# Performance work log

Measured on AMD Instinct MI355X. Metric: run time of the kernel, lower is better.

The kernel has to match this reference:

```python
import jax, jax.numpy as jnp
import numpy as np

N_AGENTS = 8
N_ENEMIES = 8
N_ALLIES = 7
H = 64            # rnn_hidden_dim (must be 64: Encoder latent dim hardcoded to 64, fed to fc3)
HEADS = 2         # hpn_head_num
OUT_NORMAL = 6    # output_normal_actions
N_ACTIONS = OUT_NORMAL + N_ENEMIES  # 14, required by expand_as in original code
E_DIM = 8
A_DIM = 8
OWN_DIM = 30
HYPER = 64        # hpn_hyper_dim
ENC_HID = 128     # predict_net_dim
BS = 2048


def _gru_cell(x, h, Wih, Whh, bih, bhh):
    # torch GRUCell math, gate order (r, z, n)
    gi = x @ Wih + bih
    gh = h @ Whh + bhh
    ir, iz, inn = jnp.split(gi, 3, axis=-1)
    hr, hz, hn = jnp.split(gh, 3, axis=-1)
    r = jax.nn.sigmoid(ir + hr)
    z = jax.nn.sigmoid(iz + hz)
    n = jnp.tanh(inn + r * hn)
    return (1.0 - z) * n + z * h


def setup_inputs() -> dict:
    key = jax.random.key(0)
    ks = jax.random.split(key, 48)
    B = BS * N_AGENTS

    def w(k, shape):
        return jax.random.normal(k, shape, dtype=jnp.float32) * 0.05

    he_out = ((E_DIM + 1) * H + 1) * HEADS   # 1154
    ha_out = A_DIM * H * HEADS               # 1024 (non-MMM map)

    return {
        "bs": BS,
        "own_feats": jax.random.normal(ks[0], (B, OWN_DIM), jnp.float32),
        "enemy_feats": jax.random.normal(ks[1], (B * N_ENEMIES, E_DIM), jnp.float32),
        "ally_feats": jax.random.normal(ks[2], (B * N_ALLIES, A_DIM), jnp.float32),
        "agent_ids": jax.random.randint(ks[3], (B,), 0, N_AGENTS),
        "last_action_ids": jax.random.randint(ks[4], (B,), 0, N_ACTIONS),
        "hidden_state": jax.random.normal(ks[5], (B, H), jnp.float32) * 0.1,
        "fc1_own_W": w(ks[6], (OWN_DIM, H)), "fc1_own_b": w(ks[7], (H,)),
        "agent_emb": w(ks[8], (N_AGENTS, H)),
        "action_emb": w(ks[9], (N_ACTIONS, H)),
        "he_W1": w(ks[10], (E_DIM, HYPER)), "he_b1": w(ks[11], (HYPER,)),
        "he_W2": w(ks[12], (HYPER, he_out)), "he_b2": w(ks[13], (he_out,)),
        "ha_W1": w(ks[14], (A_DIM, HYPER)), "ha_b1": w(ks[15], (HYPER,)),
        "ha_W2": w(ks[16], (HYPER, ha_out)), "ha_b2": w(ks[17], (ha_out,)),
        "merger_in_w": jnp.ones((1, HEADS, H), jnp.float32),
        "merger_out_w": jnp.ones((1, HEADS, 1), jnp.float32),
        "gru_Wih": w(ks[18], (H, 3 * H)), "gru_Whh": w(ks[19], (H, 3 * H)),
        "gru_bih": w(ks[20], (3 * H,)), "gru_bhh": w(ks[21], (3 * H,)),
        "fc2n_W": w(ks[22], (H, OUT_NORMAL)), "fc2n_b": w(ks[23], (OUT_NORMAL,)),
        "fc1b_W": w(ks[24], (OWN_DIM, H)), "fc1b_b": w(ks[25], (H,)),
        "gru2_Wih": w(ks[26], (H, 3 * H)), "gru2_Whh": w(ks[27], (H, 3 * H)),
        "gru2_bih": w(ks[28], (3 * H,)), "gru2_bhh": w(ks[29], (3 * H,)),
        "enc_W1": w(ks[30], (H, ENC_HID)), "enc_b1": w(ks[31], (ENC_HID,)),
        "enc_W2": w(ks[32], (ENC_HID, H)), "enc_b2": w(ks[33], (H,)),
        "fc3_W": w(ks[34], (H, N_ACTIONS)), "fc3_b": w(ks[35], (N_ACTIONS,)),
        "mlp_W": w(ks[36], (N_AGENTS, H, N_ACTIONS)), "mlp_b": w(ks[37], (N_AGENTS, N_ACTIONS)),
    }


def reference(bs, own_feats, enemy_feats, ally_feats, agent_ids, last_action_ids,
              hidden_state, fc1_own_W, fc1_own_b, agent_emb, action_emb,
              he_W1, he_b1, he_W2, he_b2, ha_W1, ha_b1, ha_W2, ha_b2,
              merger_in_w, merger_out_w, gru_Wih, gru_Whh, gru_bih, gru_bhh,
              fc2n_W, fc2n_b, fc1b_W, fc1b_b, gru2_Wih, gru2_Whh, gru2_bih, gru2_bhh,
              enc_W1, enc_b1, enc_W2, enc_b2, fc3_W, fc3_b, mlp_W, mlp_b):
    B = bs * N_AGENTS

    # own embedding + id/action embeddings
    emb_own = own_feats @ fc1_own_W + fc1_own_b
    emb_own = emb_own + agent_emb[agent_ids] + action_emb[last_action_ids]

    # hypernet-generated per-enemy fc1 weights, applied per entity, summed over enemies
    he = jax.nn.relu(enemy_feats @ he_W1 + he_b1) @ he_W2 + he_b2  # [B*E, 1154]
    cut = (H + 1) * HEADS
    w1e = he[:, :-cut].reshape(-1, E_DIM, H * HEADS)               # [B*E, e_dim, H*heads]
    emb_en = jnp.einsum('nd,ndk->nk', enemy_feats, w1e)
    emb_en = emb_en.reshape(B, N_ENEMIES, HEADS, H).sum(axis=1)    # [B, heads, H]

    ha = jax.nn.relu(ally_feats @ ha_W1 + ha_b1) @ ha_W2 + ha_b2   # [B*A, 1024]
    w1a = ha.reshape(-1, A_DIM, H * HEADS)
    emb_al = jnp.einsum('nd,ndk->nk', ally_feats, w1a)
    emb_al = emb_al.reshape(B, N_ALLIES, HEADS, H).sum(axis=1)     # [B, heads, H]

    # Merger over heads (softmax-weighted sum)
    mw = jax.nn.softmax(merger_in_w, axis=1)                       # [1, heads, H]
    merged = jnp.sum(mw * (emb_en + emb_al), axis=1)               # [B, H]

    x = jax.nn.relu(emb_own + merged)
    hh = _gru_cell(x, hidden_state, gru_Wih, gru_Whh, gru_bih, gru_bhh)  # [B, H]

    q_normal = (hh @ fc2n_W + fc2n_b).reshape(bs, N_AGENTS, OUT_NORMAL)

    # hypernet-generated attack output heads
    w2 = he[:, -cut:-HEADS].reshape(B, N_ENEMIES, H, HEADS)
    w2 = w2.transpose(0, 2, 1, 3).reshape(B, H, N_ENEMIES * HEADS)
    b2 = he[:, -HEADS:].reshape(B, N_ENEMIES * HEADS)
    qa = jnp.einsum('bh,bhk->bk', hh, w2) + b2                     # [B, E*heads]
    qa = qa.reshape(B * N_ENEMIES, HEADS)
    mo = jax.nn.softmax(merger_out_w[:, :, 0], axis=1)             # [1, heads]
    q_attack = jnp.sum(mo * qa, axis=1).reshape(bs, N_AGENTS, N_ENEMIES)

    q = jnp.concatenate([q_normal, q_attack], axis=-1)             # [bs, n_agents, 14]

    # parallel fc1 -> single-step GRU -> encoder branch
    x2 = jax.nn.relu(own_feats @ fc1b_W + fc1b_b)                  # [B, H]
    g = _gru_cell(x2, hidden_state, gru2_Wih, gru2_Whh, gru2_bih, gru2_bhh)  # [B, H]
    z = jax.nn.relu(g @ enc_W1 + enc_b1) @ enc_W2 + enc_b2         # [B, 64] encoder latent
    q_f = (z @ fc3_W + fc3_b).reshape(bs, N_AGENTS, N_ACTIONS)

    # per-agent mlps applied to first n_agents rows of gru output (as in original)
    ga = g[:N_AGENTS]                                              # [n_agents, H]
    local_q = jnp.einsum('ah,ahk->ak', ga, mlp_W) + mlp_b          # [n_agents, n_actions]
    local_qe = jnp.broadcast_to(local_q[None], q.shape)

    q_total = q + local_qe + q_f
    return (q_total, hh.reshape(bs, N_AGENTS, H), local_qe, q_f)
```

## Files before the change

kernel.cpp:

```cpp
#include <hip/hip_runtime.h>

#define HH_OFF 229376
#define LQE_OFF 1277952
#define QF_OFF 1507328

#define WB_HE 0
#define WB_HA 17408
#define WS_ATT 34816
#define WS_BATT 38912
#define WS_BH 38976
#define WS_BC 39040
#define WS_LQ 39056
#define WS_G1 39168
#define WS_G2 63744
#define WS_E1 88320
#define WS_E2 96512
#define WS_F1 104704
#define WS_END 108800

#define AWAVE 2448
#define ASAMP 336
#define TA_SH 552
#define BSTR 384

using s8v = __attribute__((ext_vector_type(8))) short;
using f4v = __attribute__((ext_vector_type(4))) float;

struct Params {
  const float *own, *ef, *af, *hid;
  const int *aid, *lid;
  const float *fc1oW, *fc1ob, *aemb, *actemb;
  const float *heW1, *heb1, *heW2, *heb2;
  const float *haW1, *hab1, *haW2, *hab2;
  const float *mi, *mo;
  const float *gWih, *gWhh, *gbih, *gbhh;
  const float *fc2nW, *fc2nb;
  const float *fc1bW, *fc1bb;
  const float *g2Wih, *g2Whh, *g2bih, *g2bhh;
  const float *eW1, *eb1, *eW2, *eb2;
  const float *fc3W, *fc3b;
  const float *mlpW, *mlpb;
};

__device__ __forceinline__ float sigm(float x) {
  x = fminf(fmaxf(x, -30.f), 30.f);
  return 1.f / (1.f + __expf(-x));
}
__device__ __forceinline__ float tanh_(float x) {
  x = fminf(fmaxf(x, -15.f), 15.f);
  float e = __expf(-2.f * x);
  return (1.f - e) / (1.f + e);
}
__device__ __forceinline__ unsigned short f2bf(float f) {
  unsigned u = __float_as_uint(f);
  return (unsigned short)((u + 0x7FFFu + ((u >> 16) & 1u)) >> 16);
}

__device__ __forceinline__ float hefold(const Params& p, int t, int h, float mw0, float mw1) {
  if (t < 512) {
    int d = t >> 6, j = t & 63;
    return mw0 * p.heW2[j * 1154 + d * 128 + h] + mw1 * p.heW2[j * 1154 + d * 128 + 64 + h];
  }
  if (t < 520) {
    int d = t - 512;
    return mw0 * p.heb2[d * 128 + h] + mw1 * p.heb2[d * 128 + 64 + h];
  }
  return 0.f;
}
__device__ __forceinline__ float hafold(const Params& p, int t, int h, float mw0, float mw1) {
  if (t < 512) {
    int d = t >> 6, j = t & 63;
    return mw0 * p.haW2[j * 1024 + d * 128 + h] + mw1 * p.haW2[j * 1024 + d * 128 + 64 + h];
  }
  if (t < 520) {
    int d = t - 512;
    return mw0 * p.hab2[d * 128 + h] + mw1 * p.hab2[d * 128 + 64 + h];
  }
  return 0.f;
}

__global__ void __launch_bounds__(512) prep_kernel(Params p, float* __restrict__ ws) {
  const int tid = threadIdx.x;
  if (blockIdx.x == 0) {
    __shared__ float g8[8][64];
    __shared__ float x2s[8][64];
    const int w = __builtin_amdgcn_readfirstlane(tid >> 6);
    const int lane = tid & 63;
    {
      float acc = p.fc1bb[lane];
      const float* ow = p.own + w * 30;
      for (int d = 0; d < 30; ++d) acc += ow[d] * p.fc1bW[d * 64 + lane];
      x2s[w][lane] = fmaxf(acc, 0.f);
      float a0 = p.g2bih[lane], a1 = p.g2bih[64 + lane], a2 = p.g2bih[128 + lane];
      float b0 = p.g2bhh[lane], b1 = p.g2bhh[64 + lane], b2 = p.g2bhh[128 + lane];
      const float* hidw = p.hid + w * 64;
      for (int k = 0; k < 64; ++k) {
        float xk = x2s[w][k];
        float hk = hidw[k];
        a0 += xk * p.g2Wih[k * 192 + lane];
        a1 += xk * p.g2Wih[k * 192 + 64 + lane];
        a2 += xk * p.g2Wih[k * 192 + 128 + lane];
        b0 += hk * p.g2Whh[k * 192 + lane];
        b1 += hk * p.g2Whh[k * 192 + 64 + lane];
        b2 += hk * p.g2Whh[k * 192 + 128 + lane];
      }
      float r = sigm(a0 + b0), z = sigm(a1 + b1);
      float n = tanh_(a2 + r * b2);
      g8[w][lane] = (1.f - z) * n + z * hidw[lane];
    }
    __syncthreads();
    if (tid < 112) {
      int a = tid / 14, c = tid % 14;
      float lacc = p.mlpb[a * 14 + c];
      for (int h = 0; h < 64; ++h) lacc += g8[a][h] * p.mlpW[(a * 64 + h) * 14 + c];
      ws[WS_LQ + tid] = lacc;
    }
    return;
  }
  const int idx = (int)(blockIdx.x - 1) * 512 + tid;
  if (idx >= WS_END) return;
  const float mo0 = sigm(p.mo[0] - p.mo[1]);
  const float mo1 = 1.f - mo0;
  if (idx < 34816) {
    int rel = (idx < WB_HA) ? idx : idx - WB_HA;
    int jp = rel & 3, lane = (rel >> 2) & 63, rest = rel >> 8;
    int nc = rest & 3, ks = rest >> 2;
    int t0 = ks * 32 + ((lane >> 4) << 3) + jp * 2;
    int h = nc * 16 + (lane & 15);
    float mw0 = sigm(p.mi[h] - p.mi[64 + h]);
    float mw1 = 1.f - mw0;
    float v0, v1;
    if (idx < WB_HA) {
      v0 = hefold(p, t0, h, mw0, mw1);
      v1 = hefold(p, t0 + 1, h, mw0, mw1);
    } else {
      v0 = hafold(p, t0, h, mw0, mw1);
      v1 = hafold(p, t0 + 1, h, mw0, mw1);
    }
    unsigned pk = (unsigned)f2bf(v0) | ((unsigned)f2bf(v1) << 16);
    ws[idx] = __uint_as_float(pk);
  } else if (idx < 38912) {
    int rel = idx - WS_ATT;
    int c = rel >> 8, rem = rel & 255, j = rem >> 2, q = rel & 3;
    int h = c * 4 + q;
    ws[idx] = mo0 * p.heW2[j * 1154 + 1024 + 2 * h] + mo1 * p.heW2[j * 1154 + 1024 + 2 * h + 1];
  } else if (idx < 38976) {
    int j = idx - WS_BATT;
    ws[idx] = mo0 * p.heW2[j * 1154 + 1152] + mo1 * p.heW2[j * 1154 + 1153];
  } else if (idx < 39040) {
    int h = idx - WS_BH;
    ws[idx] = mo0 * p.heb2[1024 + 2 * h] + mo1 * p.heb2[1024 + 2 * h + 1];
  } else if (idx == WS_BC) {
    ws[idx] = mo0 * p.heb2[1152] + mo1 * p.heb2[1153];
  } else if (idx < WS_G1) {
    return;
  } else if (idx < WS_G2) {
    int rel = idx - WS_G1;
    int k4 = rel / 1536, r2 = rel % 1536;
    int j = r2 >> 8, lane = (r2 & 255) >> 2, q = rel & 3;
    int row = 4 * k4 + q;
    ws[idx] = (j < 3) ? p.gWih[row * 192 + j * 64 + lane]
                      : p.gWhh[row * 192 + (j - 3) * 64 + lane];
  } else if (idx < WS_E1) {
    int rel = idx - WS_G2;
    int k4 = rel / 1536, r2 = rel % 1536;
    int j = r2 >> 8, lane = (r2 & 255) >> 2, q = rel & 3;
    int row = 4 * k4 + q;
    ws[idx] = (j < 3) ? p.g2Wih[row * 192 + j * 64 + lane]
                      : p.g2Whh[row * 192 + (j - 3) * 64 + lane];
  } else if (idx < WS_E2) {
    int rel = idx - WS_E1;
    int k4 = rel >> 9, j = (rel >> 8) & 1, lane = (rel & 255) >> 2, q = rel & 3;
    int row = 4 * k4 + q;
    ws[idx] = p.eW1[row * 128 + j * 64 + lane];
  } else if (idx < WS_F1) {
    int rel = idx - WS_E2;
    int k4 = rel >> 8, lane = (rel & 255) >> 2, q = rel & 3;
    int row = 4 * k4 + q;
    ws[idx] = p.eW2[row * 64 + lane];
  } else {
    int rel = idx - WS_F1;
    int k4 = rel >> 9, j = (rel >> 8) & 1, lane = (rel & 255) >> 2, q = rel & 3;
    int row = 4 * k4 + q;
    float v;
    if (row < 30) v = (j == 0) ? p.fc1oW[row * 64 + lane] : p.fc1bW[row * 64 + lane];
    else if (row == 30) v = (j == 0) ? p.fc1ob[lane] : p.fc1bb[lane];
    else v = 0.f;
    ws[idx] = v;
  }
}

__global__ void __launch_bounds__(256, 2) kernelA(Params p, const float* __restrict__ ws,
                                                  float* __restrict__ out) {
  __shared__ float smem[4 * AWAVE];
  const int w = __builtin_amdgcn_readfirstlane((int)(threadIdx.x >> 6));
  const int lane = threadIdx.x & 63;
  float* S = &smem[w * AWAVE];
  unsigned short* ta = (unsigned short*)S;
  float* SB = S + 1104;
  const int i0 = blockIdx.x * 16 + w * 4;

  if (lane < 24) {
#pragma unroll
    for (int m = 0; m < 4; ++m) ta[m * TA_SH + 520 + lane] = 0;
  }
#pragma unroll
  for (int s = 0; s < 4; ++s) {
    SB[s * ASAMP + 208 + lane] = p.ef[(i0 + s) * 64 + lane];
    if (lane < 56) SB[s * ASAMP + 272 + lane] = p.af[(i0 + s) * 56 + lane];
  }
  {
    float w1[8];
#pragma unroll
    for (int d = 0; d < 8; ++d) w1[d] = p.heW1[d * 64 + lane];
    const float b1 = p.heb1[lane];
#pragma unroll
    for (int s = 0; s < 4; ++s) {
      float T[8], fs[8];
#pragma unroll
      for (int d = 0; d < 8; ++d) { T[d] = 0.f; fs[d] = 0.f; }
#pragma unroll
      for (int e = 0; e < 8; ++e) {
        float4 a = *(const float4*)&SB[s * ASAMP + 208 + e * 8];
        float4 b = *(const float4*)&SB[s * ASAMP + 208 + e * 8 + 4];
        float acc = b1 + a.x * w1[0] + a.y * w1[1] + a.z * w1[2] + a.w * w1[3] +
                    b.x * w1[4] + b.y * w1[5] + b.z * w1[6] + b.w * w1[7];
        float r = fmaxf(acc, 0.f);
        T[0] += r * a.x; T[1] += r * a.y; T[2] += r * a.z; T[3] += r * a.w;
        T[4] += r * b.x; T[5] += r * b.y; T[6] += r * b.z; T[7] += r * b.w;
        fs[0] += a.x; fs[1] += a.y; fs[2] += a.z; fs[3] += a.w;
        fs[4] += b.x; fs[5] += b.y; fs[6] += b.z; fs[7] += b.w;
      }
#pragma unroll
      for (int d = 0; d < 8; ++d) ta[s * TA_SH + d * 64 + lane] = f2bf(T[d]);
      if (lane == 0) {
#pragma unroll
        for (int d = 0; d < 8; ++d) ta[s * TA_SH + 512 + d] = f2bf(fs[d]);
      }
    }
  }
  f4v acc[4];
#pragma unroll
  for (int nc = 0; nc < 4; ++nc) acc[nc] = (f4v){0.f, 0.f, 0.f, 0.f};
  {
    const s8v* WB = (const s8v*)(ws + WB_HE);
    for (int ks = 0; ks < 17; ++ks) {
      s8v a = *(const s8v*)&ta[(lane & 3) * TA_SH + ks * 32 + ((lane >> 4) << 3)];
#pragma unroll
      for (int nc = 0; nc < 4; ++nc) {
        s8v b = WB[(ks * 4 + nc) * 64 + lane];
        acc[nc] = __builtin_amdgcn_mfma_f32_16x16x32_bf16(a, b, acc[nc], 0, 0, 0);
      }
    }
  }
  {
    float w1[8];
#pragma unroll
    for (int d = 0; d < 8; ++d) w1[d] = p.haW1[d * 64 + lane];
    const float b1 = p.hab1[lane];
#pragma unroll
    for (int s = 0; s < 4; ++s) {
      float T[8], fs[8];
#pragma unroll
      for (int d = 0; d < 8; ++d) { T[d] = 0.f; fs[d] = 0.f; }
#pragma unroll
      for (int e = 0; e < 7; ++e) {
        float4 a = *(const float4*)&SB[s * ASAMP + 272 + e * 8];
        float4 b = *(const float4*)&SB[s * ASAMP + 272 + e * 8 + 4];
        float acc2 = b1 + a.x * w1[0] + a.y * w1[1] + a.z * w1[2] + a.w * w1[3] +
                     b.x * w1[4] + b.y * w1[5] + b.z * w1[6] + b.w * w1[7];
        float r = fmaxf(acc2, 0.f);
        T[0] += r * a.x; T[1] += r * a.y; T[2] += r * a.z; T[3] += r * a.w;
        T[4] += r * b.x; T[5] += r * b.y; T[6] += r * b.z; T[7] += r * b.w;
        fs[0] += a.x; fs[1] += a.y; fs[2] += a.z; fs[3] += a.w;
        fs[4] += b.x; fs[5] += b.y; fs[6] += b.z; fs[7] += b.w;
      }
#pragma unroll
      for (int d = 0; d < 8; ++d) ta[s * TA_SH + d * 64 + lane] = f2bf(T[d]);
      if (lane == 0) {
#pragma unroll
        for (int d = 0; d < 8; ++d) ta[s * TA_SH + 512 + d] = f2bf(fs[d]);
      }
    }
  }
  {
    const s8v* WB = (const s8v*)(ws + WB_HA);
    for (int ks = 0; ks < 17; ++ks) {
      s8v a = *(const s8v*)&ta[(lane & 3) * TA_SH + ks * 32 + ((lane >> 4) << 3)];
#pragma unroll
      for (int nc = 0; nc < 4; ++nc) {
        s8v b = WB[(ks * 4 + nc) * 64 + lane];
        acc[nc] = __builtin_amdgcn_mfma_f32_16x16x32_bf16(a, b, acc[nc], 0, 0, 0);
      }
    }
  }
  if (lane < 16) {
#pragma unroll
    for (int nc = 0; nc < 4; ++nc) {
#pragma unroll
      for (int r = 0; r < 4; ++r) SB[r * ASAMP + nc * 16 + lane] = acc[nc][r];
    }
  }
#pragma unroll
  for (int s = 0; s < 4; ++s) {
    SB[s * ASAMP + 64 + lane] = p.hid[(i0 + s) * 64 + lane];
    if (lane < 32)
      SB[s * ASAMP + 272 + lane] =
          (lane < 30) ? p.own[(i0 + s) * 30 + lane] : (lane == 30 ? 1.f : 0.f);
  }
  {
    float aO[4] = {0.f, 0.f, 0.f, 0.f};
    const float4* F = (const float4*)(ws + WS_F1);
    for (int k4 = 0; k4 < 8; ++k4) {
      float4 wo = F[k4 * 128 + lane];
#pragma unroll
      for (int s = 0; s < 4; ++s) {
        float4 o4 = *(const float4*)&SB[s * ASAMP + 272 + k4 * 4];
        aO[s] += o4.x * wo.x + o4.y * wo.y + o4.z * wo.z + o4.w * wo.w;
      }
    }
#pragma unroll
    for (int s = 0; s < 4; ++s) {
      const int i = i0 + s;
      float mer = SB[s * ASAMP + lane];
      float x = aO[s] + p.aemb[p.aid[i] * 64 + lane] + p.actemb[p.lid[i] * 64 + lane] + mer;
      SB[s * ASAMP + lane] = fmaxf(x, 0.f);
    }
  }
  {
    const float bi0 = p.gbih[lane] + p.gbhh[lane];
    const float bi1 = p.gbih[64 + lane] + p.gbhh[64 + lane];
    const float bi2i = p.gbih[128 + lane];
    const float bi2h = p.gbhh[128 + lane];
    float A0[4], A1[4], A2[4], B2[4];
#pragma unroll
    for (int s = 0; s < 4; ++s) { A0[s] = bi0; A1[s] = bi1; A2[s] = bi2i; B2[s] = bi2h; }
    const float4* G = (const float4*)(ws + WS_G1);
    for (int k4 = 0; k4 < 16; ++k4) {
      float4 w0 = G[k4 * 384 + lane];
      float4 w1v = G[k4 * 384 + 64 + lane];
      float4 w2v = G[k4 * 384 + 128 + lane];
      float4 w3 = G[k4 * 384 + 192 + lane];
      float4 w4v = G[k4 * 384 + 256 + lane];
      float4 w5 = G[k4 * 384 + 320 + lane];
#pragma unroll
      for (int s = 0; s < 4; ++s) {
        float4 x4 = *(const float4*)&SB[s * ASAMP + k4 * 4];
        float4 h4 = *(const float4*)&SB[s * ASAMP + 64 + k4 * 4];
        A0[s] += x4.x * w0.x + x4.y * w0.y + x4.z * w0.z + x4.w * w0.w +
                 h4.x * w3.x + h4.y * w3.y + h4.z * w3.z + h4.w * w3.w;
        A1[s] += x4.x * w1v.x + x4.y * w1v.y + x4.z * w1v.z + x4.w * w1v.w +
                 h4.x * w4v.x + h4.y * w4v.y + h4.z * w4v.z + h4.w * w4v.w;
        A2[s] += x4.x * w2v.x + x4.y * w2v.y + x4.z * w2v.z + x4.w * w2v.w;
        B2[s] += h4.x * w5.x + h4.y * w5.y + h4.z * w5.z + h4.w * w5.w;
      }
    }
#pragma unroll
    for (int s = 0; s < 4; ++s) {
      float r = sigm(A0[s]);
      float z = sigm(A1[s]);
      float n = tanh_(A2[s] + r * B2[s]);
      float hp = SB[s * ASAMP + 64 + lane];
      float hh = (1.f - z) * n + z * hp;
      SB[s * ASAMP + 128 + lane] = hh;
      out[HH_OFF + (i0 + s) * 64 + lane] = hh;
    }
  }
  {
    float v4[4];
    const float batt = ws[WS_BATT + lane];
#pragma unroll
    for (int s = 0; s < 4; ++s) v4[s] = batt;
    const float4* A4 = (const float4*)(ws + WS_ATT);
    for (int c = 0; c < 16; ++c) {
      float4 wv = A4[c * 64 + lane];
#pragma unroll
      for (int s = 0; s < 4; ++s) {
        float4 h4 = *(const float4*)&SB[s * ASAMP + 128 + c * 4];
        v4[s] += h4.x * wv.x + h4.y * wv.y + h4.z * wv.z + h4.w * wv.w;
      }
    }
    float w1[8];
#pragma unroll
    for (int d = 0; d < 8; ++d) w1[d] = p.heW1[d * 64 + lane];
    const float b1 = p.heb1[lane];
    const float bhv = ws[WS_BH + lane];
    const float bc = ws[WS_BC];
#pragma unroll
    for (int s = 0; s < 4; ++s) {
      float red[9];
#pragma unroll
      for (int e = 0; e < 8; ++e) {
        float4 a = *(const float4*)&SB[s * ASAMP + 208 + e * 8];
        float4 b = *(const float4*)&SB[s * ASAMP + 208 + e * 8 + 4];
        float acc2 = b1 + a.x * w1[0] + a.y * w1[1] + a.z * w1[2] + a.w * w1[3] +
                     b.x * w1[4] + b.y * w1[5] + b.z * w1[6] + b.w * w1[7];
        red[e] = fmaxf(acc2, 0.f) * v4[s];
      }
      red[8] = SB[s * ASAMP + 128 + lane] * bhv;
#pragma unroll
      for (int off = 32; off >= 1; off >>= 1) {
#pragma unroll
        for (int t = 0; t < 9; ++t) red[t] += __shfl_xor(red[t], off, 64);
      }
      if (lane == 0) {
#pragma unroll
        for (int e = 0; e < 8; ++e) SB[s * ASAMP + 192 + 6 + e] = red[e] + red[8] + bc;
      }
    }
  }
  if (lane < 56) {
    const int s = lane / 14, c = lane % 14;
    const int i = i0 + s;
    float qo;
    if (c < 6) {
      float a2 = p.fc2nb[c];
      for (int h = 0; h < 64; ++h) a2 += SB[s * ASAMP + 128 + h] * p.fc2nW[h * 6 + c];
      qo = a2;
    } else {
      qo = SB[s * ASAMP + 192 + c];
    }
    float lq = ws[WS_LQ + (i & 7) * 14 + c];
    out[i * 14 + c] = qo + lq;
    out[LQE_OFF + i * 14 + c] = lq;
  }
}

__global__ void __launch_bounds__(256, 2) kernelB(Params p, const float* __restrict__ ws,
                                                  float* __restrict__ out) {
  __shared__ float smem[4 * 4 * BSTR];
  const int w = __builtin_amdgcn_readfirstlane((int)(threadIdx.x >> 6));
  const int lane = threadIdx.x & 63;
  float* S = &smem[w * 4 * BSTR];
  const int i0 = blockIdx.x * 16 + w * 4;

#pragma unroll
  for (int s = 0; s < 4; ++s) {
    S[s * BSTR + 64 + lane] = p.hid[(i0 + s) * 64 + lane];
    if (lane < 32)
      S[s * BSTR + 192 + lane] =
          (lane < 30) ? p.own[(i0 + s) * 30 + lane] : (lane == 30 ? 1.f : 0.f);
  }
  {
    float aB[4] = {0.f, 0.f, 0.f, 0.f};
    const float4* F = (const float4*)(ws + WS_F1);
    for (int k4 = 0; k4 < 8; ++k4) {
      float4 wb = F[k4 * 128 + 64 + lane];
#pragma unroll
      for (int s = 0; s < 4; ++s) {
        float4 o4 = *(const float4*)&S[s * BSTR + 192 + k4 * 4];
        aB[s] += o4.x * wb.x + o4.y * wb.y + o4.z * wb.z + o4.w * wb.w;
      }
    }
#pragma unroll
    for (int s = 0; s < 4; ++s) S[s * BSTR + lane] = fmaxf(aB[s], 0.f);
  }
  {
    const float bi0 = p.g2bih[lane] + p.g2bhh[lane];
    const float bi1 = p.g2bih[64 + lane] + p.g2bhh[64 + lane];
    const float bi2i = p.g2bih[128 + lane];
    const float bi2h = p.g2bhh[128 + lane];
    float A0[4], A1[4], A2[4], B2[4];
#pragma unroll
    for (int s = 0; s < 4; ++s) { A0[s] = bi0; A1[s] = bi1; A2[s] = bi2i; B2[s] = bi2h; }
    const float4* G = (const float4*)(ws + WS_G2);
    for (int k4 = 0; k4 < 16; ++k4) {
      float4 w0 = G[k4 * 384 + lane];
      float4 w1v = G[k4 * 384 + 64 + lane];
      float4 w2v = G[k4 * 384 + 128 + lane];
      float4 w3 = G[k4 * 384 + 192 + lane];
      float4 w4v = G[k4 * 384 + 256 + lane];
      float4 w5 = G[k4 * 384 + 320 + lane];
#pragma unroll
      for (int s = 0; s < 4; ++s) {
        float4 x4 = *(const float4*)&S[s * BSTR + k4 * 4];
        float4 h4 = *(const float4*)&S[s * BSTR + 64 + k4 * 4];
        A0[s] += x4.x * w0.x + x4.y * w0.y + x4.z * w0.z + x4.w * w0.w +
                 h4.x * w3.x + h4.y * w3.y + h4.z * w3.z + h4.w * w3.w;
        A1[s] += x4.x * w1v.x + x4.y * w1v.y + x4.z * w1v.z + x4.w * w1v.w +
                 h4.x * w4v.x + h4.y * w4v.y + h4.z * w4v.z + h4.w * w4v.w;
        A2[s] += x4.x * w2v.x + x4.y * w2v.y + x4.z * w2v.z + x4.w * w2v.w;
        B2[s] += h4.x * w5.x + h4.y * w5.y + h4.z * w5.z + h4.w * w5.w;
      }
    }
#pragma unroll
    for (int s = 0; s < 4; ++s) {
      float r = sigm(A0[s]);
      float z = sigm(A1[s]);
      float n = tanh_(A2[s] + r * B2[s]);
      float hp = S[s * BSTR + 64 + lane];
      S[s * BSTR + 128 + lane] = (1.f - z) * n + z * hp;
    }
  }
  {
    float C0[4], C1[4];
#pragma unroll
    for (int s = 0; s < 4; ++s) { C0[s] = p.eb1[lane]; C1[s] = p.eb1[64 + lane]; }
    const float4* E1 = (const float4*)(ws + WS_E1);
    for (int k4 = 0; k4 < 16; ++k4) {
      float4 w0 = E1[k4 * 128 + lane];
      float4 w1v = E1[k4 * 128 + 64 + lane];
#pragma unroll
      for (int s = 0; s < 4; ++s) {
        float4 g4 = *(const float4*)&S[s * BSTR + 128 + k4 * 4];
        C0[s] += g4.x * w0.x + g4.y * w0.y + g4.z * w0.z + g4.w * w0.w;
        C1[s] += g4.x * w1v.x + g4.y * w1v.y + g4.z * w1v.z + g4.w * w1v.w;
      }
    }
#pragma unroll
    for (int s = 0; s < 4; ++s) {
      S[s * BSTR + 192 + lane] = fmaxf(C0[s], 0.f);
      S[s * BSTR + 256 + lane] = fmaxf(C1[s], 0.f);
    }
  }
  {
    float Z[4];
#pragma unroll
    for (int s = 0; s < 4; ++s) Z[s] = p.eb2[lane];
    const float4* E2 = (const float4*)(ws + WS_E2);
    for (int k4 = 0; k4 < 32; ++k4) {
      float4 wv = E2[k4 * 64 + lane];
#pragma unroll
      for (int s = 0; s < 4; ++s) {
        float4 z4 = *(const float4*)&S[s * BSTR + 192 + k4 * 4];
        Z[s] += z4.x * wv.x + z4.y * wv.y + z4.z * wv.z + z4.w * wv.w;
      }
    }
#pragma unroll
    for (int s = 0; s < 4; ++s) S[s * BSTR + 320 + lane] = Z[s];
  }
  if (lane < 56) {
    const int s = lane / 14, c = lane % 14;
    const int i = i0 + s;
    float qf = p.fc3b[c];
    for (int k = 0; k < 64; ++k) qf += S[s * BSTR + 320 + k] * p.fc3W[k * 14 + c];
    out[QF_OFF + i * 14 + c] = qf;
    out[i * 14 + c] += qf;
  }
}

extern "C" void kernel_launch(void* const* d_in, const int* in_sizes, int n_in,
                              void* d_out, int out_size, void* d_ws, size_t ws_size,
                              hipStream_t stream) {
  (void)in_sizes; (void)n_in; (void)out_size; (void)ws_size;
  Params p;
  p.own = (const float*)d_in[1];
  p.ef = (const float*)d_in[2];
  p.af = (const float*)d_in[3];
  p.aid = (const int*)d_in[4];
  p.lid = (const int*)d_in[5];
  p.hid = (const float*)d_in[6];
  p.fc1oW = (const float*)d_in[7];
  p.fc1ob = (const float*)d_in[8];
  p.aemb = (const float*)d_in[9];
  p.actemb = (const float*)d_in[10];
  p.heW1 = (const float*)d_in[11];
  p.heb1 = (const float*)d_in[12];
  p.heW2 = (const float*)d_in[13];
  p.heb2 = (const float*)d_in[14];
  p.haW1 = (const float*)d_in[15];
  p.hab1 = (const float*)d_in[16];
  p.haW2 = (const float*)d_in[17];
  p.hab2 = (const float*)d_in[18];
  p.mi = (const float*)d_in[19];
  p.mo = (const float*)d_in[20];
  p.gWih = (const float*)d_in[21];
  p.gWhh = (const float*)d_in[22];
  p.gbih = (const float*)d_in[23];
  p.gbhh = (const float*)d_in[24];
  p.fc2nW = (const float*)d_in[25];
  p.fc2nb = (const float*)d_in[26];
  p.fc1bW = (const float*)d_in[27];
  p.fc1bb = (const float*)d_in[28];
  p.g2Wih = (const float*)d_in[29];
  p.g2Whh = (const float*)d_in[30];
  p.g2bih = (const float*)d_in[31];
  p.g2bhh = (const float*)d_in[32];
  p.eW1 = (const float*)d_in[33];
  p.eb1 = (const float*)d_in[34];
  p.eW2 = (const float*)d_in[35];
  p.eb2 = (const float*)d_in[36];
  p.fc3W = (const float*)d_in[37];
  p.fc3b = (const float*)d_in[38];
  p.mlpW = (const float*)d_in[39];
  p.mlpb = (const float*)d_in[40];
  float* ws = (float*)d_ws;
  float* out = (float*)d_out;
  prep_kernel<<<dim3(214), dim3(512), 0, stream>>>(p, ws);
  kernelA<<<dim3(1024), dim3(256), 0, stream>>>(p, ws, out);
  kernelB<<<dim3(1024), dim3(256), 0, stream>>>(p, ws, out);
}
```

Baseline: 272.4 us.

## Fuse kernelA and kernelB into one kernel sharing loads and LDS

Merges the hypernetwork/GRU kernel and the parallel fc1/GRU/encoder kernel into one launch. The hidden state is loaded once, and the fc1b projection reuses the own-feature tile already in LDS. The final output is written once instead of being read-modify-written by a second kernel. This removes one launch plus redundant global traffic, at the cost of a longer serial per-wave chain, higher register pressure and a slightly larger LDS footprint.

```diff
diff --git a/kernel.cpp b/kernel.cpp
--- a/kernel.cpp
+++ b/kernel.cpp
@@ -18,10 +18,10 @@
 #define WS_F1 104704
 #define WS_END 108800
 
-#define AWAVE 2448
-#define ASAMP 336
+#define ASAMP 344
 #define TA_SH 552
-#define BSTR 384
+#define TFS 276
+#define AWAVE 2480
 
 using s8v = __attribute__((ext_vector_type(8))) short;
 using f4v = __attribute__((ext_vector_type(4))) float;
@@ -190,15 +190,17 @@
   }
 }
 
-__global__ void __launch_bounds__(256, 2) kernelA(Params p, const float* __restrict__ ws,
-                                                  float* __restrict__ out) {
+__global__ void __launch_bounds__(256, 2) mainK(Params p, const float* __restrict__ ws,
+                                                float* __restrict__ out) {
   __shared__ float smem[4 * AWAVE];
   const int w = __builtin_amdgcn_readfirstlane((int)(threadIdx.x >> 6));
   const int lane = threadIdx.x & 63;
   float* S = &smem[w * AWAVE];
   unsigned short* ta = (unsigned short*)S;
+  float* TF = S;
   float* SB = S + 1104;
   const int i0 = blockIdx.x * 16 + w * 4;
+  const int quad = lane >> 4;
 
   if (lane < 24) {
 #pragma unroll
@@ -207,6 +209,7 @@
 #pragma unroll
   for (int s = 0; s < 4; ++s) {
     SB[s * ASAMP + 208 + lane] = p.ef[(i0 + s) * 64 + lane];
+    SB[s * ASAMP + 64 + lane] = p.hid[(i0 + s) * 64 + lane];
     if (lane < 56) SB[s * ASAMP + 272 + lane] = p.af[(i0 + s) * 56 + lane];
   }
   {
@@ -245,12 +248,11 @@
   {
     const s8v* WB = (const s8v*)(ws + WB_HE);
     for (int ks = 0; ks < 17; ++ks) {
-      s8v a = *(const s8v*)&ta[(lane & 3) * TA_SH + ks * 32 + ((lane >> 4) << 3)];
-#pragma unroll
-      for (int nc = 0; nc < 4; ++nc) {
-        s8v b = WB[(ks * 4 + nc) * 64 + lane];
-        acc[nc] = __builtin_amdgcn_mfma_f32_16x16x32_bf16(a, b, acc[nc], 0, 0, 0);
-      }
+      s8v a = *(const s8v*)&ta[(lane & 3) * TA_SH + ks * 32 + quad * 8];
+#pragma unroll
+      for (int nc = 0; nc < 4; ++nc)
+        acc[nc] = __builtin_amdgcn_mfma_f32_16x16x32_bf16(a, WB[(ks * 4 + nc) * 64 + lane],
+                                                          acc[nc], 0, 0, 0);
     }
   }
   {
@@ -286,12 +288,11 @@
   {
     const s8v* WB = (const s8v*)(ws + WB_HA);
     for (int ks = 0; ks < 17; ++ks) {
-      s8v a = *(const s8v*)&ta[(lane & 3) * TA_SH + ks * 32 + ((lane >> 4) << 3)];
-#pragma unroll
-      for (int nc = 0; nc < 4; ++nc) {
-        s8v b = WB[(ks * 4 + nc) * 64 + lane];
-        acc[nc] = __builtin_amdgcn_mfma_f32_16x16x32_bf16(a, b, acc[nc], 0, 0, 0);
-      }
+      s8v a = *(const s8v*)&ta[(lane & 3) * TA_SH + ks * 32 + quad * 8];
+#pragma unroll
+      for (int nc = 0; nc < 4; ++nc)
+        acc[nc] = __builtin_amdgcn_mfma_f32_16x16x32_bf16(a, WB[(ks * 4 + nc) * 64 + lane],
+                                                          acc[nc], 0, 0, 0);
     }
   }
   if (lane < 16) {
@@ -303,20 +304,21 @@
   }
 #pragma unroll
   for (int s = 0; s < 4; ++s) {
-    SB[s * ASAMP + 64 + lane] = p.hid[(i0 + s) * 64 + lane];
     if (lane < 32)
       SB[s * ASAMP + 272 + lane] =
           (lane < 30) ? p.own[(i0 + s) * 30 + lane] : (lane == 30 ? 1.f : 0.f);
   }
   {
-    float aO[4] = {0.f, 0.f, 0.f, 0.f};
+    float aO[4] = {0.f, 0.f, 0.f, 0.f}, aB[4] = {0.f, 0.f, 0.f, 0.f};
     const float4* F = (const float4*)(ws + WS_F1);
     for (int k4 = 0; k4 < 8; ++k4) {
       float4 wo = F[k4 * 128 + lane];
+      float4 wb = F[k4 * 128 + 64 + lane];
 #pragma unroll
       for (int s = 0; s < 4; ++s) {
         float4 o4 = *(const float4*)&SB[s * ASAMP + 272 + k4 * 4];
         aO[s] += o4.x * wo.x + o4.y * wo.y + o4.z * wo.z + o4.w * wo.w;
+        aB[s] += o4.x * wb.x + o4.y * wb.y + o4.z * wb.z + o4.w * wb.w;
       }
     }
 #pragma unroll
@@ -325,6 +327,7 @@
       float mer = SB[s * ASAMP + lane];
       float x = aO[s] + p.aemb[p.aid[i] * 64 + lane] + p.actemb[p.lid[i] * 64 + lane] + mer;
       SB[s * ASAMP + lane] = fmaxf(x, 0.f);
+      TF[s * TFS + lane] = fmaxf(aB[s], 0.f);
     }
   }
   {
@@ -409,52 +412,6 @@
       }
     }
   }
-  if (lane < 56) {
-    const int s = lane / 14, c = lane % 14;
-    const int i = i0 + s;
-    float qo;
-    if (c < 6) {
-      float a2 = p.fc2nb[c];
-      for (int h = 0; h < 64; ++h) a2 += SB[s * ASAMP + 128 + h] * p.fc2nW[h * 6 + c];
-      qo = a2;
-    } else {
-      qo = SB[s * ASAMP + 192 + c];
-    }
-    float lq = ws[WS_LQ + (i & 7) * 14 + c];
-    out[i * 14 + c] = qo + lq;
-    out[LQE_OFF + i * 14 + c] = lq;
-  }
-}
-
-__global__ void __launch_bounds__(256, 2) kernelB(Params p, const float* __restrict__ ws,
-                                                  float* __restrict__ out) {
-  __shared__ float smem[4 * 4 * BSTR];
-  const int w = __builtin_amdgcn_readfirstlane((int)(threadIdx.x >> 6));
-  const int lane = threadIdx.x & 63;
-  float* S = &smem[w * 4 * BSTR];
-  const int i0 = blockIdx.x * 16 + w * 4;
-
-#pragma unroll
-  for (int s = 0; s < 4; ++s) {
-    S[s * BSTR + 64 + lane] = p.hid[(i0 + s) * 64 + lane];
-    if (lane < 32)
-      S[s * BSTR + 192 + lane] =
-          (lane < 30) ? p.own[(i0 + s) * 30 + lane] : (lane == 30 ? 1.f : 0.f);
-  }
-  {
-    float aB[4] = {0.f, 0.f, 0.f, 0.f};
-    const float4* F = (const float4*)(ws + WS_F1);
-    for (int k4 = 0; k4 < 8; ++k4) {
-      float4 wb = F[k4 * 128 + 64 + lane];
-#pragma unroll
-      for (int s = 0; s < 4; ++s) {
-        float4 o4 = *(const float4*)&S[s * BSTR + 192 + k4 * 4];
-        aB[s] += o4.x * wb.x + o4.y * wb.y + o4.z * wb.z + o4.w * wb.w;
-      }
-    }
-#pragma unroll
-    for (int s = 0; s < 4; ++s) S[s * BSTR + lane] = fmaxf(aB[s], 0.f);
-  }
   {
     const float bi0 = p.g2bih[lane] + p.g2bhh[lane];
     const float bi1 = p.g2bih[64 + lane] + p.g2bhh[64 + lane];
@@ -473,8 +430,8 @@
       float4 w5 = G[k4 * 384 + 320 + lane];
 #pragma unroll
       for (int s = 0; s < 4; ++s) {
-        float4 x4 = *(const float4*)&S[s * BSTR + k4 * 4];
-        float4 h4 = *(const float4*)&S[s * BSTR + 64 + k4 * 4];
+        float4 x4 = *(const float4*)&TF[s * TFS + k4 * 4];
+        float4 h4 = *(const float4*)&SB[s * ASAMP + 64 + k4 * 4];
         A0[s] += x4.x * w0.x + x4.y * w0.y + x4.z * w0.z + x4.w * w0.w +
                  h4.x * w3.x + h4.y * w3.y + h4.z * w3.z + h4.w * w3.w;
         A1[s] += x4.x * w1v.x + x4.y * w1v.y + x4.z * w1v.z + x4.w * w1v.w +
@@ -488,8 +445,8 @@
       float r = sigm(A0[s]);
       float z = sigm(A1[s]);
       float n = tanh_(A2[s] + r * B2[s]);
-      float hp = S[s * BSTR + 64 + lane];
-      S[s * BSTR + 128 + lane] = (1.f - z) * n + z * hp;
+      float hp = SB[s * ASAMP + 64 + lane];
+      TF[s * TFS + 64 + lane] = (1.f - z) * n + z * hp;
     }
   }
   {
@@ -502,15 +459,15 @@
       float4 w1v = E1[k4 * 128 + 64 + lane];
 #pragma unroll
       for (int s = 0; s < 4; ++s) {
-        float4 g4 = *(const float4*)&S[s * BSTR + 128 + k4 * 4];
+        float4 g4 = *(const float4*)&TF[s * TFS + 64 + k4 * 4];
         C0[s] += g4.x * w0.x + g4.y * w0.y + g4.z * w0.z + g4.w * w0.w;
         C1[s] += g4.x * w1v.x + g4.y * w1v.y + g4.z * w1v.z + g4.w * w1v.w;
       }
     }
 #pragma unroll
     for (int s = 0; s < 4; ++s) {
-      S[s * BSTR + 192 + lane] = fmaxf(C0[s], 0.f);
-      S[s * BSTR + 256 + lane] = fmaxf(C1[s], 0.f);
+      TF[s * TFS + 128 + lane] = fmaxf(C0[s], 0.f);
+      TF[s * TFS + 192 + lane] = fmaxf(C1[s], 0.f);
     }
   }
   {
@@ -522,20 +479,30 @@
       float4 wv = E2[k4 * 64 + lane];
 #pragma unroll
       for (int s = 0; s < 4; ++s) {
-        float4 z4 = *(const float4*)&S[s * BSTR + 192 + k4 * 4];
+        float4 z4 = *(const float4*)&TF[s * TFS + 128 + k4 * 4];
         Z[s] += z4.x * wv.x + z4.y * wv.y + z4.z * wv.z + z4.w * wv.w;
       }
     }
 #pragma unroll
-    for (int s = 0; s < 4; ++s) S[s * BSTR + 320 + lane] = Z[s];
+    for (int s = 0; s < 4; ++s) TF[s * TFS + lane] = Z[s];
   }
   if (lane < 56) {
     const int s = lane / 14, c = lane % 14;
     const int i = i0 + s;
     float qf = p.fc3b[c];
-    for (int k = 0; k < 64; ++k) qf += S[s * BSTR + 320 + k] * p.fc3W[k * 14 + c];
+    for (int k = 0; k < 64; ++k) qf += TF[s * TFS + k] * p.fc3W[k * 14 + c];
+    float qo;
+    if (c < 6) {
+      float a2 = p.fc2nb[c];
+      for (int h = 0; h < 64; ++h) a2 += SB[s * ASAMP + 128 + h] * p.fc2nW[h * 6 + c];
+      qo = a2;
+    } else {
+      qo = SB[s * ASAMP + 192 + c];
+    }
+    float lq = ws[WS_LQ + (i & 7) * 14 + c];
+    out[i * 14 + c] = qo + lq + qf;
+    out[LQE_OFF + i * 14 + c] = lq;
     out[QF_OFF + i * 14 + c] = qf;
-    out[i * 14 + c] += qf;
   }
 }
 
@@ -587,6 +554,5 @@
   float* ws = (float*)d_ws;
   float* out = (float*)d_out;
   prep_kernel<<<dim3(214), dim3(512), 0, stream>>>(p, ws);
-  kernelA<<<dim3(1024), dim3(256), 0, stream>>>(p, ws, out);
-  kernelB<<<dim3(1024), dim3(256), 0, stream>>>(p, ws, out);
-}
+  mainK<<<dim3(1024), dim3(256), 0, stream>>>(p, ws, out);
+}
```

Measured after the change: 275.7 us. Within noise of the previous version (+1.2%).
